# Performance work log

Hardware: AMD Instinct MI355X
Metric: run time of the kernel (lower is better)

The kernel has to match this reference:

```python
import jax, jax.numpy as jnp
import numpy as np
from jax import lax

B, C, D, H, W = 2, 256, 32, 64, 192
TRAIN_W = 640
DISPS = np.arange(D, dtype=np.float32) * 0.01  # norm_disp_range


def conv1x1(x, w, b):
    # x [B,Cin,H,W], w [Cout,Cin]
    return jnp.einsum('bchw,oc->bohw', x, w) + b[None, :, None, None]


def conv3x3(x, w, b):
    y = lax.conv_general_dilated(x, w, (1, 1), 'SAME',
                                 dimension_numbers=('NCHW', 'OIHW', 'NCHW'))
    return y + b[None, :, None, None]


def warp_volume(x, shift_px):
    """Horizontal bilinear warp with border clamp for each disparity.
    x [B,Cc,H,W], shift_px [B,D] (pixel shift) -> [B,Cc,D,H,W]."""
    Wd = x.shape[3]
    j = jnp.arange(Wd, dtype=x.dtype)
    src = jnp.clip(j[None, None, :] + shift_px[:, :, None], 0.0, Wd - 1.0)  # [B,D,W]
    x0 = jnp.floor(src).astype(jnp.int32)
    x1 = jnp.minimum(x0 + 1, Wd - 1)
    frac = src - x0.astype(src.dtype)  # [B,D,W]

    def one(xb, i0, i1, fb):
        g0 = xb[:, :, i0]  # [Cc,H,D,W]
        g1 = xb[:, :, i1]
        out = g0 * (1.0 - fb) + g1 * fb
        return out.transpose(0, 2, 1, 3)  # [Cc,D,H,W]

    return jax.vmap(one)(x, x0, x1, frac)


def setup_inputs() -> dict:
    key = jax.random.key(0)
    ks = jax.random.split(key, 16)
    f32 = jnp.float32
    inp = {
        't_feat': jax.random.normal(ks[0], (B, C, H, W), f32),
        's_feat': jax.random.normal(ks[1], (B, C, H, W), f32),
        'directs': jnp.ones((B, 1, 1, 1), f32),
        'qw': jax.random.normal(ks[2], (C // 4, C), f32) * 0.05,
        'qb': jax.random.normal(ks[3], (C // 4,), f32) * 0.05,
        'kw': jax.random.normal(ks[4], (C // 4, C), f32) * 0.05,
        'kb': jax.random.normal(ks[5], (C // 4,), f32) * 0.05,
        'vw': jax.random.normal(ks[6], (C // 4, C), f32) * 0.05,
        'vb': jax.random.normal(ks[7], (C // 4,), f32) * 0.05,
        'p1w': jax.random.normal(ks[8], (C // 4, C // 2, 3, 3), f32) * 0.05,
        'p1b': jax.random.normal(ks[9], (C // 4,), f32) * 0.05,
        'p2w': jax.random.normal(ks[10], (D, C // 4, 3, 3), f32) * 0.05,
        'p2b': jax.random.normal(ks[11], (D,), f32) * 0.05,
        'rw': jax.random.normal(ks[12], (C, C + D), f32) * 0.05,
        'rb': jax.random.normal(ks[13], (C,), f32) * 0.05,
        'img_w': TRAIN_W,
    }
    return inp


def reference(t_feat, s_feat, directs, qw, qb, kw, kb, vw, vb,
              p1w, p1b, p2w, p2b, rw, rb, img_w):
    rel_scale = (TRAIN_W / img_w) if img_w != TRAIN_W else 1.0
    q = conv1x1(t_feat, qw, qb)  # [B,C/4,H,W]
    k = conv1x1(s_feat, kw, kb)
    v = conv1x1(s_feat, vw, vb)

    Wd = t_feat.shape[3]
    disps = jnp.asarray(DISPS, t_feat.dtype)
    # normalized shift d*2*rel_scale*directs -> pixels: * (W-1)/2
    shift = disps[None, :] * rel_scale * directs.reshape(-1, 1) * (Wd - 1)  # [B,D]

    wk = warp_volume(k, shift)  # [B,C/4,D,H,W]
    wv = warp_volume(v, shift)

    cq = q.shape[1]
    cost = jnp.einsum('bchw,bcdhw->bdhw', q, wk) / (cq ** 0.5)  # [B,D,H,W]
    norm_cost = jax.nn.softmax(cost, axis=1)
    agg_v = jnp.einsum('bdhw,bcdhw->bchw', norm_cost, wv)  # [B,C/4,H,W]

    h1 = jax.nn.elu(conv3x3(jnp.concatenate([q, agg_v], axis=1), p1w, p1b))
    res_cost = conv3x3(h1, p2w, p2b)  # [B,D,H,W]
    cost = (cost + res_cost) * 0.5
    norm_cost = jax.nn.softmax(cost, axis=1)
    x = jax.nn.elu(conv1x1(jnp.concatenate([t_feat, norm_cost], axis=1), rw, rb))
    return x, cost
```

## Files before the change

### kernel.cpp

```cpp
#include <hip/hip_runtime.h>

#define BB 2
#define CC 256
#define CQ 64
#define DD 32
#define HH 64
#define WW 192
#define HW (HH*WW)
#define NPIX (BB*HW)

typedef __attribute__((ext_vector_type(8))) short bf16x8;
typedef __attribute__((ext_vector_type(4))) float f32x4;

__device__ __forceinline__ float b2f(ushort s){ return __uint_as_float(((uint)s)<<16); }
__device__ __forceinline__ ushort f2b(float f){
    uint u = __float_as_uint(f);
    return (ushort)((u + 0x7fffu + ((u>>16)&1u)) >> 16);
}
__device__ __forceinline__ float eluf(float v){ return v > 0.f ? v : (__expf(v)-1.f); }

__global__ __launch_bounds__(256) void k_prep_feat(
    const float* __restrict__ t_feat, const float* __restrict__ s_feat,
    ushort* __restrict__ Tt, ushort* __restrict__ Ts)
{
    __shared__ ushort sT[64*264];
    int blk = blockIdx.x;
    int which = blk / 384;
    int rem   = blk % 384;
    int b     = rem / 192;
    int tile  = rem % 192;
    int p0    = tile*64;
    const float* src = which ? s_feat : t_feat;
    ushort* dst      = which ? Ts : Tt;
    int tid = threadIdx.x;

    for (int i = tid; i < 2048; i += 256){
        int px  = i & 63;
        int c16 = i >> 6;
        const float* p = src + ((size_t)(b*CC + c16*8))*HW + p0 + px;
        uint u[4];
        #pragma unroll
        for (int j2=0;j2<4;++j2)
            u[j2] = (uint)f2b(p[(size_t)(2*j2)*HW]) | ((uint)f2b(p[(size_t)(2*j2+1)*HW])<<16);
        uint4 q4; q4.x=u[0]; q4.y=u[1]; q4.z=u[2]; q4.w=u[3];
        *(uint4*)&sT[(px*33 + c16)*8] = q4;
    }
    __syncthreads();
    for (int i = tid; i < 2048; i += 256){
        int c16 = i & 31;
        int px  = i >> 5;
        uint4 v = *(const uint4*)&sT[(px*33 + c16)*8];
        *(uint4*)(dst + ((size_t)(b*HW + p0 + px))*CC + c16*8) = v;
    }
}

__global__ __launch_bounds__(256) void k_prep_w(
    const float* __restrict__ qw, const float* __restrict__ qb,
    const float* __restrict__ kw, const float* __restrict__ kb,
    const float* __restrict__ vw, const float* __restrict__ vb,
    const float* __restrict__ p1w, const float* __restrict__ p2w,
    const float* __restrict__ rw,
    ushort* __restrict__ Wqkv, float* __restrict__ bqkv,
    ushort* __restrict__ A1, ushort* __restrict__ A2, ushort* __restrict__ Ar)
{
    int id = blockIdx.x*256 + threadIdx.x;
    if (id < 49152) {
        int o = id / 256, c = id % 256;
        float v = (o<64)? qw[o*256+c] : (o<128)? kw[(o-64)*256+c] : vw[(o-128)*256+c];
        Wqkv[id] = f2b(v);
    } else if (id < 49344) {
        int o = id - 49152;
        bqkv[o] = (o<64)? qb[o] : (o<128)? kb[o-64] : vb[o-128];
    } else if (id < 49344+73728) {
        int i = id - 49344;
        int o = i/1152, r = i%1152, t = r/128, ci = r%128;
        A1[i] = f2b(p1w[(size_t)(o*128+ci)*9 + t]);
    } else if (id < 49344+73728+18432) {
        int i = id - (49344+73728);
        int o = i/576, r = i%576, t = r/64, ci = r%64;
        A2[i] = f2b(p2w[(size_t)(o*64+ci)*9 + t]);
    } else if (id < 49344+73728+18432+73728) {
        int i = id - (49344+73728+18432);
        Ar[i] = f2b(rw[i]);
    }
}

__global__ __launch_bounds__(256) void g_qkv(
    const ushort* __restrict__ Tt, const ushort* __restrict__ Ts,
    const ushort* __restrict__ Wqkv, const float* __restrict__ bqkv,
    ushort* __restrict__ X1, ushort* __restrict__ Vb)
{
    __shared__ ushort sT[32*264];
    __shared__ ushort sS[32*264];
    int tid = threadIdx.x;
    int bid = blockIdx.x;
    int tile = (bid & 7)*96 + (bid >> 3);
    int p0 = tile * 32;

    for (int i = tid; i < 1024; i += 256){
        int px = i >> 5, c16 = i & 31;
        size_t gsrc = ((size_t)(p0 + px))*CC + c16*8;
        *(uint4*)&sT[(px*33 + c16)*8] = *(const uint4*)(Tt + gsrc);
        *(uint4*)&sS[(px*33 + c16)*8] = *(const uint4*)(Ts + gsrc);
    }
    __syncthreads();

    int wv = tid >> 6, lane = tid & 63;
    int lm = lane & 15, lk = lane >> 4;
    f32x4 acc[3][2];
    #pragma unroll
    for (int g=0;g<3;++g){ acc[g][0]=(f32x4){0.f,0.f,0.f,0.f}; acc[g][1]=(f32x4){0.f,0.f,0.f,0.f}; }
    const ushort* Ap = Wqkv + (size_t)(wv*16 + lm)*CC + lk*8;

    #pragma unroll
    for (int k0=0; k0<CC; k0+=32){
        bf16x8 a0 = *(const bf16x8*)(Ap + k0);
        bf16x8 a1 = *(const bf16x8*)(Ap + 64*CC + k0);
        bf16x8 a2 = *(const bf16x8*)(Ap + 128*CC + k0);
        #pragma unroll
        for (int nt=0; nt<2; ++nt){
            int ch = (nt*16+lm)*33 + (k0>>3) + lk;
            bf16x8 bT = *(const bf16x8*)&sT[ch*8];
            bf16x8 bS = *(const bf16x8*)&sS[ch*8];
            acc[0][nt] = __builtin_amdgcn_mfma_f32_16x16x32_bf16(a0, bT, acc[0][nt], 0,0,0);
            acc[1][nt] = __builtin_amdgcn_mfma_f32_16x16x32_bf16(a1, bS, acc[1][nt], 0,0,0);
            acc[2][nt] = __builtin_amdgcn_mfma_f32_16x16x32_bf16(a2, bS, acc[2][nt], 0,0,0);
        }
    }
    int ol = wv*16 + lk*4;
    #pragma unroll
    for (int g=0;g<3;++g){
        int ob = g*64 + ol;
        #pragma unroll
        for (int nt=0; nt<2; ++nt){
            int p = p0 + nt*16 + lm;
            uint u0 = (uint)f2b(acc[g][nt][0]+bqkv[ob])   | ((uint)f2b(acc[g][nt][1]+bqkv[ob+1])<<16);
            uint u1 = (uint)f2b(acc[g][nt][2]+bqkv[ob+2]) | ((uint)f2b(acc[g][nt][3]+bqkv[ob+3])<<16);
            ushort* dst;
            if (g==0)      dst = X1 + (size_t)p*128 + ol;
            else if (g==1) dst = X1 + (size_t)p*128 + 64 + ol;
            else           dst = Vb + (size_t)p*64 + ol;
            *(uint2*)dst = make_uint2(u0, u1);
        }
    }
}

#define SVS 193
__global__ __launch_bounds__(512) void k_ca(
    const ushort* __restrict__ X1, const ushort* __restrict__ Vb,
    const float* __restrict__ directs, const int* __restrict__ img_w_p,
    float* __restrict__ C1, ushort* __restrict__ Agg)
{
    __shared__ ushort sK[8*SVS*8];
    __shared__ ushort sV[8*SVS*8];
    int tid = threadIdx.x;
    int j   = blockIdx.x;
    int r8  = j & 7;
    int kk  = j >> 3;
    int sub = kk % 6;
    int rhi = kk / 6;
    int row = rhi*8 + r8;
    int b   = row >> 6;
    int h   = row & 63;
    int w0  = sub * 32;
    size_t rowbase = (size_t)b*HW + (size_t)h*WW;

    for (int i = tid; i < 1536; i += 512){
        int c8 = i & 7, x = i >> 3;
        *(uint4*)&sK[(c8*SVS + x)*8] = *(const uint4*)(X1 + (rowbase+x)*128 + 64 + c8*8);
        *(uint4*)&sV[(c8*SVS + x)*8] = *(const uint4*)(Vb + (rowbase+x)*64 + c8*8);
    }
    __syncthreads();

    int px  = tid >> 4;
    int l16 = tid & 15;
    int oct = l16 >> 1;
    int dh  = l16 & 1;
    int w   = w0 + px;
    size_t n = rowbase + w;

    int imw = img_w_p[0];
    float rel = (imw != 640) ? (640.0f/(float)imw) : 1.0f;
    float sf = 0.01f * rel * directs[b] * 191.0f;
    float wf = (float)w;

    float qf[8];
    {
        bf16x8 qv = *(const bf16x8*)(X1 + n*128 + oct*8);
        #pragma unroll
        for (int j2=0;j2<8;++j2) qf[j2] = b2f((ushort)qv[j2]);
    }

    float cost[16]; int x0k[16]; float frk[16];
    #pragma unroll
    for (int k=0;k<16;++k){
        int d = dh*16 + k;
        float srcx = fminf(fmaxf(wf + (float)d*sf, 0.f), 191.0f);
        int x0 = (int)floorf(srcx);
        int x1 = min(x0+1, 191);
        float fr = srcx - (float)x0;
        x0k[k] = x0; frk[k] = fr;
        bf16x8 k0v = *(const bf16x8*)&sK[(oct*SVS + x0)*8];
        bf16x8 k1v = *(const bf16x8*)&sK[(oct*SVS + x1)*8];
        float s0 = 0.f, s1 = 0.f;
        #pragma unroll
        for (int j2=0;j2<8;++j2){
            s0 += qf[j2]*b2f((ushort)k0v[j2]);
            s1 += qf[j2]*b2f((ushort)k1v[j2]);
        }
        cost[k] = s0 + fr*(s1-s0);
    }
    #pragma unroll
    for (int k=0;k<16;++k){
        float v = cost[k];
        v += __shfl_xor(v, 2);
        v += __shfl_xor(v, 4);
        v += __shfl_xor(v, 8);
        cost[k] = v * 0.125f;
    }
    if (oct == 0){
        float* cp = C1 + n*DD + dh*16;
        #pragma unroll
        for (int q=0;q<4;++q){
            f32x4 t4; t4[0]=cost[q*4]; t4[1]=cost[q*4+1]; t4[2]=cost[q*4+2]; t4[3]=cost[q*4+3];
            *(f32x4*)(cp + q*4) = t4;
        }
    }
    float mm = cost[0];
    #pragma unroll
    for (int k=1;k<16;++k) mm = fmaxf(mm, cost[k]);
    mm = fmaxf(mm, __shfl_xor(mm, 1));
    float ss = 0.f;
    #pragma unroll
    for (int k=0;k<16;++k){ cost[k] = __expf(cost[k]-mm); ss += cost[k]; }
    ss += __shfl_xor(ss, 1);
    float inv = 1.f/ss;

    float agg[8];
    #pragma unroll
    for (int j2=0;j2<8;++j2) agg[j2]=0.f;
    #pragma unroll
    for (int k=0;k<16;++k){
        float pd = cost[k]*inv;
        int x0 = x0k[k];
        int x1 = min(x0+1, 191);
        float fr = frk[k];
        float a1 = pd*fr, a0 = pd - a1;
        bf16x8 v0v = *(const bf16x8*)&sV[(oct*SVS + x0)*8];
        bf16x8 v1v = *(const bf16x8*)&sV[(oct*SVS + x1)*8];
        #pragma unroll
        for (int j2=0;j2<8;++j2)
            agg[j2] += a0*b2f((ushort)v0v[j2]) + a1*b2f((ushort)v1v[j2]);
    }
    #pragma unroll
    for (int j2=0;j2<8;++j2) agg[j2] += __shfl_xor(agg[j2], 1);
    if (dh == 0){
        uint u[4];
        #pragma unroll
        for (int j2=0;j2<4;++j2)
            u[j2] = (uint)f2b(agg[j2*2]) | ((uint)f2b(agg[j2*2+1])<<16);
        uint4 q4; q4.x=u[0]; q4.y=u[1]; q4.z=u[2]; q4.w=u[3];
        *(uint4*)(Agg + n*64 + oct*8) = q4;
    }
}

__global__ __launch_bounds__(256) void g_conv1(
    const ushort* __restrict__ X1, const ushort* __restrict__ Agg,
    const ushort* __restrict__ A1, const float* __restrict__ p1b,
    ushort* __restrict__ X2)
{
    __shared__ ushort sB[3*16*34*8];
    int tid = threadIdx.x;
    int wv = tid >> 6, lane = tid & 63;
    int lm = lane & 15, lk = lane >> 4;
    int bid = blockIdx.x;
    int tile = (bid & 7)*96 + (bid >> 3);
    int n0 = tile * 32;
    int b  = n0 / HW;
    int pl = n0 % HW;
    int h  = pl / WW, w0 = pl % WW;

    for (int i = tid; i < 1632; i += 256){
        int dh = i / 544, rem2 = i % 544;
        int c16 = rem2 / 34, x = rem2 % 34;
        int hh = h + dh - 1, wx = w0 + x - 1;
        uint4 val = make_uint4(0,0,0,0);
        if (hh >= 0 && hh < HH && wx >= 0 && wx < WW){
            size_t pix = (size_t)b*HW + (size_t)hh*WW + wx;
            val = (c16 < 8) ? *(const uint4*)(X1 + pix*128 + c16*8)
                            : *(const uint4*)(Agg + pix*64 + (c16-8)*8);
        }
        *(uint4*)&sB[((dh*16 + c16)*34 + x)*8] = val;
    }
    __syncthreads();

    int mw = wv & 1, nw = wv >> 1;
    const ushort* Ap = A1 + (size_t)(mw*32 + lm)*1152 + lk*8;
    f32x4 acc0 = {0.f,0.f,0.f,0.f}, acc1 = {0.f,0.f,0.f,0.f};
    int xb = nw*16 + lm;
    #pragma unroll
    for (int t=0; t<9; ++t){
        int dh = t/3, dw = t%3;
        #pragma unroll
        for (int c0=0; c0<128; c0+=32){
            bf16x8 bb = *(const bf16x8*)&sB[((dh*16 + (c0>>3)+lk)*34 + xb + dw)*8];
            bf16x8 a0 = *(const bf16x8*)(Ap + t*128 + c0);
            bf16x8 a1 = *(const bf16x8*)(Ap + (size_t)16*1152 + t*128 + c0);
            acc0 = __builtin_amdgcn_mfma_f32_16x16x32_bf16(a0, bb, acc0, 0,0,0);
            acc1 = __builtin_amdgcn_mfma_f32_16x16x32_bf16(a1, bb, acc1, 0,0,0);
        }
    }
    int pg = n0 + nw*16 + lm;
    int o0 = mw*32 + lk*4;
    {
        uint u0 = (uint)f2b(eluf(acc0[0]+p1b[o0]))   | ((uint)f2b(eluf(acc0[1]+p1b[o0+1]))<<16);
        uint u1 = (uint)f2b(eluf(acc0[2]+p1b[o0+2])) | ((uint)f2b(eluf(acc0[3]+p1b[o0+3]))<<16);
        *(uint2*)(X2 + (size_t)pg*64 + o0) = make_uint2(u0, u1);
        int o1 = o0 + 16;
        uint u2 = (uint)f2b(eluf(acc1[0]+p1b[o1]))   | ((uint)f2b(eluf(acc1[1]+p1b[o1+1]))<<16);
        uint u3 = (uint)f2b(eluf(acc1[2]+p1b[o1+2])) | ((uint)f2b(eluf(acc1[3]+p1b[o1+3]))<<16);
        *(uint2*)(X2 + (size_t)pg*64 + o1) = make_uint2(u2, u3);
    }
}

__global__ __launch_bounds__(256) void g_conv2(
    const ushort* __restrict__ X2, const ushort* __restrict__ A2,
    const float* __restrict__ p2b, const float* __restrict__ C1,
    float* __restrict__ cost_out)
{
    __shared__ ushort sB[3*8*34*8];
    int tid = threadIdx.x;
    int wv = tid >> 6, lane = tid & 63;
    int lm = lane & 15, lk = lane >> 4;
    int bid = blockIdx.x;
    int tile = (bid & 7)*96 + (bid >> 3);
    int n0 = tile * 32;
    int b  = n0 / HW;
    int pl = n0 % HW;
    int h  = pl / WW, w0 = pl % WW;

    for (int i = tid; i < 816; i += 256){
        int dh = i / 272, rem2 = i % 272;
        int c16 = rem2 / 34, x = rem2 % 34;
        int hh = h + dh - 1, wx = w0 + x - 1;
        uint4 val = make_uint4(0,0,0,0);
        if (hh >= 0 && hh < HH && wx >= 0 && wx < WW)
            val = *(const uint4*)(X2 + ((size_t)b*HW + (size_t)hh*WW + wx)*64 + c16*8);
        *(uint4*)&sB[((dh*8 + c16)*34 + x)*8] = val;
    }
    __syncthreads();

    int mw = wv & 1, nw = wv >> 1;
    const ushort* Ap = A2 + (size_t)(mw*16 + lm)*576 + lk*8;
    f32x4 acc = {0.f,0.f,0.f,0.f};
    int xb = nw*16 + lm;
    #pragma unroll
    for (int t=0; t<9; ++t){
        int dh = t/3, dw = t%3;
        #pragma unroll
        for (int c0=0; c0<64; c0+=32){
            bf16x8 bb = *(const bf16x8*)&sB[((dh*8 + (c0>>3)+lk)*34 + xb + dw)*8];
            bf16x8 a  = *(const bf16x8*)(Ap + t*64 + c0);
            acc = __builtin_amdgcn_mfma_f32_16x16x32_bf16(a, bb, acc, 0,0,0);
        }
    }
    int pg = n0 + nw*16 + lm;
    int pll = pg % HW;
    int o = mw*16 + lk*4;
    f32x4 cv = *(const f32x4*)(C1 + (size_t)pg*DD + o);
    #pragma unroll
    for (int j=0;j<4;++j)
        cost_out[((size_t)(b*DD + o + j))*HW + pll] = (cv[j] + acc[j] + p2b[o+j]) * 0.5f;
}

__global__ __launch_bounds__(256) void k_sm2(
    const float* __restrict__ cost_out, ushort* __restrict__ NC)
{
    int n = blockIdx.x*256 + threadIdx.x;
    int b = n / HW, pl = n % HW;
    const float* cp = cost_out + (size_t)b*DD*HW + pl;
    float v[DD]; float m = -1e30f;
    #pragma unroll
    for (int d=0; d<DD; ++d){ v[d] = cp[(size_t)d*HW]; m = fmaxf(m, v[d]); }
    float s = 0.f;
    #pragma unroll
    for (int d=0; d<DD; ++d){ v[d] = __expf(v[d]-m); s += v[d]; }
    float inv = 1.f/s;
    ushort* op = NC + (size_t)n*DD;
    #pragma unroll
    for (int d8=0; d8<4; ++d8){
        uint u[4];
        #pragma unroll
        for (int j2=0;j2<4;++j2)
            u[j2] = (uint)f2b(v[d8*8+j2*2]*inv) | ((uint)f2b(v[d8*8+j2*2+1]*inv)<<16);
        uint4 q4; q4.x=u[0]; q4.y=u[1]; q4.z=u[2]; q4.w=u[3];
        *(uint4*)(op + d8*8) = q4;
    }
}

__global__ __launch_bounds__(256) void g_final(
    const ushort* __restrict__ Tt, const ushort* __restrict__ NC,
    const ushort* __restrict__ Ar, const float* __restrict__ rb,
    float* __restrict__ xout)
{
    __shared__ ushort sT[32*264];
    __shared__ ushort sN[32*40];
    int tid = threadIdx.x;
    int bid = blockIdx.x;
    int tile = (bid & 7)*96 + (bid >> 3);
    int p0 = tile * 32;

    for (int i = tid; i < 1024; i += 256){
        int px = i >> 5, c16 = i & 31;
        *(uint4*)&sT[(px*33 + c16)*8] = *(const uint4*)(Tt + ((size_t)(p0+px))*CC + c16*8);
    }
    if (tid < 128){
        int px = tid >> 2, c4 = tid & 3;
        *(uint4*)&sN[(px*5 + c4)*8] = *(const uint4*)(NC + ((size_t)(p0+px))*DD + c4*8);
    }
    __syncthreads();

    int wv = tid >> 6, lane = tid & 63;
    int lm = lane & 15, lk = lane >> 4;
    f32x4 acc[4][2];
    #pragma unroll
    for (int mi=0;mi<4;++mi){ acc[mi][0]=(f32x4){0.f,0.f,0.f,0.f}; acc[mi][1]=(f32x4){0.f,0.f,0.f,0.f}; }
    const ushort* Ap = Ar + (size_t)(wv*64 + lm)*288 + lk*8;

    #pragma unroll
    for (int k0=0; k0<288; k0+=32){
        bf16x8 a[4];
        #pragma unroll
        for (int mi=0;mi<4;++mi) a[mi] = *(const bf16x8*)(Ap + (size_t)mi*16*288 + k0);
        #pragma unroll
        for (int nt=0; nt<2; ++nt){
            int prow = nt*16 + lm;
            bf16x8 bb = (k0 < 256) ? *(const bf16x8*)&sT[(prow*33 + (k0>>3) + lk)*8]
                                   : *(const bf16x8*)&sN[(prow*5 + lk)*8];
            #pragma unroll
            for (int mi=0;mi<4;++mi)
                acc[mi][nt] = __builtin_amdgcn_mfma_f32_16x16x32_bf16(a[mi], bb, acc[mi][nt], 0,0,0);
        }
    }
    #pragma unroll
    for (int mi=0;mi<4;++mi){
        int o = wv*64 + mi*16 + lk*4;
        #pragma unroll
        for (int nt=0; nt<2; ++nt){
            int p = p0 + nt*16 + lm;
            int b = p / HW, pl = p % HW;
            #pragma unroll
            for (int j=0;j<4;++j)
                xout[((size_t)(b*CC + o + j))*HW + pl] = eluf(acc[mi][nt][j] + rb[o+j]);
        }
    }
}

extern "C" void kernel_launch(void* const* d_in, const int* in_sizes, int n_in,
                              void* d_out, int out_size, void* d_ws, size_t ws_size,
                              hipStream_t stream)
{
    const float* t_feat = (const float*)d_in[0];
    const float* s_feat = (const float*)d_in[1];
    const float* directs= (const float*)d_in[2];
    const float* qw = (const float*)d_in[3];
    const float* qb = (const float*)d_in[4];
    const float* kw = (const float*)d_in[5];
    const float* kb = (const float*)d_in[6];
    const float* vw = (const float*)d_in[7];
    const float* vb = (const float*)d_in[8];
    const float* p1w= (const float*)d_in[9];
    const float* p1b= (const float*)d_in[10];
    const float* p2w= (const float*)d_in[11];
    const float* p2b= (const float*)d_in[12];
    const float* rw = (const float*)d_in[13];
    const float* rb = (const float*)d_in[14];
    const int* img_w= (const int*)d_in[15];

    char* wsb = (char*)d_ws;
    ushort* Tt   = (ushort*)(wsb + 0);
    char*  tsreg = wsb + 12582912;
    ushort* Ts   = (ushort*)tsreg;
    ushort* X2   = (ushort*)tsreg;
    float*  C1   = (float*)(tsreg + 3145728);
    ushort* Agg  = (ushort*)(tsreg + 6291456);
    ushort* X1   = (ushort*)(wsb + 25165824);
    ushort* Vb   = (ushort*)(wsb + 31457280);
    ushort* NC   = (ushort*)(wsb + 31457280);
    ushort* Wqkv = (ushort*)(wsb + 34603008);
    float*  bqkv = (float*) (wsb + 34701312);
    ushort* A1   = (ushort*)(wsb + 34702336);
    ushort* A2   = (ushort*)(wsb + 34849792);
    ushort* Ar   = (ushort*)(wsb + 34886656);
    if (ws_size < 35034112) return;

    float* xout     = (float*)d_out;
    float* cost_out = xout + (size_t)BB*CC*HW;

    k_prep_feat<<<768, 256, 0, stream>>>(t_feat, s_feat, Tt, Ts);
    k_prep_w  <<<841,  256, 0, stream>>>(qw,qb,kw,kb,vw,vb,p1w,p2w,rw, Wqkv,bqkv,A1,A2,Ar);
    g_qkv     <<<768,  256, 0, stream>>>(Tt, Ts, Wqkv, bqkv, X1, Vb);
    k_ca      <<<768,  512, 0, stream>>>(X1, Vb, directs, img_w, C1, Agg);
    g_conv1   <<<768,  256, 0, stream>>>(X1, Agg, A1, p1b, X2);
    g_conv2   <<<768,  256, 0, stream>>>(X2, A2, p2b, C1, cost_out);
    k_sm2     <<<96,   256, 0, stream>>>(cost_out, NC);
    g_final   <<<768,  256, 0, stream>>>(Tt, NC, Ar, rb, xout);
}
```

Measured before the change: 113.4 us.

## Recast cost-volume attention as banded MFMA matmuls with scattered warp weights

The k_ca kernel now loads only a 160-column band of K and V around each 32-pixel tile into swizzled shared memory. It computes a dense Q·K score matrix with bf16 MFMA and interpolates cost per disparity from that matrix. Softmax weights are scattered via shared-memory atomics into a per-pixel column-weight matrix, and a second MFMA multiplies V by those weights to form the aggregate. This replaces scalar per-disparity dot products with matrix-core work, at the cost of extra syncs, atomics and redundant work on unused band columns. Clamping indices into the band assumes shifts stay within the band, which holds for the default disparity range.

```diff
diff --git a/kernel.cpp b/kernel.cpp
--- a/kernel.cpp
+++ b/kernel.cpp
@@ -145,14 +145,19 @@
     }
 }
 
-#define SVS 193
+#define BAND 160
+#define SROW 161
+#define PROW 168
 __global__ __launch_bounds__(512) void k_ca(
     const ushort* __restrict__ X1, const ushort* __restrict__ Vb,
     const float* __restrict__ directs, const int* __restrict__ img_w_p,
     float* __restrict__ C1, ushort* __restrict__ Agg)
 {
-    __shared__ ushort sK[8*SVS*8];
-    __shared__ ushort sV[8*SVS*8];
+    __shared__ ushort sQ[32*64];
+    __shared__ ushort sK[BAND*64];
+    __shared__ ushort sV[BAND*64];
+    __shared__ float  sS[32*SROW];
+    __shared__ ushort sPC[32*PROW];
     int tid = threadIdx.x;
     int j   = blockIdx.x;
     int r8  = j & 7;
@@ -165,102 +170,126 @@
     int w0  = sub * 32;
     size_t rowbase = (size_t)b*HW + (size_t)h*WW;
 
-    for (int i = tid; i < 1536; i += 512){
-        int c8 = i & 7, x = i >> 3;
-        *(uint4*)&sK[(c8*SVS + x)*8] = *(const uint4*)(X1 + (rowbase+x)*128 + 64 + c8*8);
-        *(uint4*)&sV[(c8*SVS + x)*8] = *(const uint4*)(Vb + (rowbase+x)*64 + c8*8);
+    for (int i = tid; i < BAND*8; i += 512){
+        int x = i >> 3, c8 = i & 7;
+        int gx = w0 - 64 + x;
+        uint4 kv = make_uint4(0,0,0,0), vv = make_uint4(0,0,0,0);
+        if (gx >= 0 && gx < WW){
+            kv = *(const uint4*)(X1 + (rowbase+gx)*128 + 64 + c8*8);
+            vv = *(const uint4*)(Vb + (rowbase+gx)*64 + c8*8);
+        }
+        int sw = (x*8 + (c8 ^ (x&7)))*8;
+        *(uint4*)&sK[sw] = kv;
+        *(uint4*)&sV[sw] = vv;
+    }
+    if (tid < 256){
+        int px = tid >> 3, c8 = tid & 7;
+        uint4 qv = *(const uint4*)(X1 + (rowbase + w0 + px)*128 + c8*8);
+        *(uint4*)&sQ[(px*8 + (c8 ^ (px&7)))*8] = qv;
+    }
+    __syncthreads();
+
+    int w8 = tid >> 6, lane = tid & 63;
+    int lm = lane & 15, lk = lane >> 4;
+
+    {
+        int mt = w8 & 1;
+        int qrow = mt*16 + lm;
+        for (int nt = (w8 >> 1); nt < 10; nt += 4){
+            int xrow = nt*16 + lm;
+            f32x4 acc = {0.f,0.f,0.f,0.f};
+            #pragma unroll
+            for (int kt=0; kt<2; ++kt){
+                bf16x8 a = *(const bf16x8*)&sQ[(qrow*8 + ((kt*4+lk) ^ (qrow&7)))*8];
+                bf16x8 bbf = *(const bf16x8*)&sK[(xrow*8 + ((kt*4+lk) ^ (xrow&7)))*8];
+                acc = __builtin_amdgcn_mfma_f32_16x16x32_bf16(a, bbf, acc, 0,0,0);
+            }
+            #pragma unroll
+            for (int jj=0; jj<4; ++jj)
+                sS[(mt*16 + lk*4 + jj)*SROW + xrow] = acc[jj];
+        }
     }
     __syncthreads();
 
     int px  = tid >> 4;
     int l16 = tid & 15;
-    int oct = l16 >> 1;
-    int dh  = l16 & 1;
     int w   = w0 + px;
     size_t n = rowbase + w;
-
     int imw = img_w_p[0];
     float rel = (imw != 640) ? (640.0f/(float)imw) : 1.0f;
     float sf = 0.01f * rel * directs[b] * 191.0f;
     float wf = (float)w;
 
-    float qf[8];
-    {
-        bf16x8 qv = *(const bf16x8*)(X1 + n*128 + oct*8);
-        #pragma unroll
-        for (int j2=0;j2<8;++j2) qf[j2] = b2f((ushort)qv[j2]);
-    }
-
-    float cost[16]; int x0k[16]; float frk[16];
-    #pragma unroll
-    for (int k=0;k<16;++k){
-        int d = dh*16 + k;
+    float cost[2]; int xi0[2], xi1[2]; float frk[2];
+    #pragma unroll
+    for (int t=0; t<2; ++t){
+        int d = l16*2 + t;
         float srcx = fminf(fmaxf(wf + (float)d*sf, 0.f), 191.0f);
         int x0 = (int)floorf(srcx);
-        int x1 = min(x0+1, 191);
+        int x1 = min(x0+1, WW-1);
         float fr = srcx - (float)x0;
-        x0k[k] = x0; frk[k] = fr;
-        bf16x8 k0v = *(const bf16x8*)&sK[(oct*SVS + x0)*8];
-        bf16x8 k1v = *(const bf16x8*)&sK[(oct*SVS + x1)*8];
-        float s0 = 0.f, s1 = 0.f;
-        #pragma unroll
-        for (int j2=0;j2<8;++j2){
-            s0 += qf[j2]*b2f((ushort)k0v[j2]);
-            s1 += qf[j2]*b2f((ushort)k1v[j2]);
-        }
-        cost[k] = s0 + fr*(s1-s0);
-    }
-    #pragma unroll
-    for (int k=0;k<16;++k){
-        float v = cost[k];
-        v += __shfl_xor(v, 2);
-        v += __shfl_xor(v, 4);
-        v += __shfl_xor(v, 8);
-        cost[k] = v * 0.125f;
-    }
-    if (oct == 0){
-        float* cp = C1 + n*DD + dh*16;
-        #pragma unroll
-        for (int q=0;q<4;++q){
-            f32x4 t4; t4[0]=cost[q*4]; t4[1]=cost[q*4+1]; t4[2]=cost[q*4+2]; t4[3]=cost[q*4+3];
-            *(f32x4*)(cp + q*4) = t4;
-        }
-    }
-    float mm = cost[0];
-    #pragma unroll
-    for (int k=1;k<16;++k) mm = fmaxf(mm, cost[k]);
+        int i0 = min(max(x0 - w0 + 64, 0), BAND-1);
+        int i1 = min(max(x1 - w0 + 64, 0), BAND-1);
+        xi0[t] = i0; xi1[t] = i1; frk[t] = fr;
+        float s0 = sS[px*SROW + i0];
+        float s1 = sS[px*SROW + i1];
+        cost[t] = (s0 + fr*(s1-s0)) * 0.125f;
+    }
+    *(float2*)(C1 + n*DD + l16*2) = make_float2(cost[0], cost[1]);
+    float mm = fmaxf(cost[0], cost[1]);
     mm = fmaxf(mm, __shfl_xor(mm, 1));
-    float ss = 0.f;
-    #pragma unroll
-    for (int k=0;k<16;++k){ cost[k] = __expf(cost[k]-mm); ss += cost[k]; }
+    mm = fmaxf(mm, __shfl_xor(mm, 2));
+    mm = fmaxf(mm, __shfl_xor(mm, 4));
+    mm = fmaxf(mm, __shfl_xor(mm, 8));
+    float e0 = __expf(cost[0]-mm), e1 = __expf(cost[1]-mm);
+    float ss = e0 + e1;
     ss += __shfl_xor(ss, 1);
+    ss += __shfl_xor(ss, 2);
+    ss += __shfl_xor(ss, 4);
+    ss += __shfl_xor(ss, 8);
     float inv = 1.f/ss;
-
-    float agg[8];
-    #pragma unroll
-    for (int j2=0;j2<8;++j2) agg[j2]=0.f;
-    #pragma unroll
-    for (int k=0;k<16;++k){
-        float pd = cost[k]*inv;
-        int x0 = x0k[k];
-        int x1 = min(x0+1, 191);
-        float fr = frk[k];
-        float a1 = pd*fr, a0 = pd - a1;
-        bf16x8 v0v = *(const bf16x8*)&sV[(oct*SVS + x0)*8];
-        bf16x8 v1v = *(const bf16x8*)&sV[(oct*SVS + x1)*8];
-        #pragma unroll
-        for (int j2=0;j2<8;++j2)
-            agg[j2] += a0*b2f((ushort)v0v[j2]) + a1*b2f((ushort)v1v[j2]);
-    }
-    #pragma unroll
-    for (int j2=0;j2<8;++j2) agg[j2] += __shfl_xor(agg[j2], 1);
-    if (dh == 0){
-        uint u[4];
-        #pragma unroll
-        for (int j2=0;j2<4;++j2)
-            u[j2] = (uint)f2b(agg[j2*2]) | ((uint)f2b(agg[j2*2+1])<<16);
-        uint4 q4; q4.x=u[0]; q4.y=u[1]; q4.z=u[2]; q4.w=u[3];
-        *(uint4*)(Agg + n*64 + oct*8) = q4;
+    float p0 = e0*inv, p1 = e1*inv;
+    __syncthreads();
+
+    for (int i = tid; i < 32*SROW; i += 512) sS[i] = 0.f;
+    __syncthreads();
+
+    {
+        float w1a = p0*frk[0], w0a = p0 - w1a;
+        float w1b = p1*frk[1], w0b = p1 - w1b;
+        atomicAdd(&sS[px*SROW + xi0[0]], w0a);
+        atomicAdd(&sS[px*SROW + xi1[0]], w1a);
+        atomicAdd(&sS[px*SROW + xi0[1]], w0b);
+        atomicAdd(&sS[px*SROW + xi1[1]], w1b);
+    }
+    __syncthreads();
+
+    #pragma unroll
+    for (int q=0; q<10; ++q){
+        int xi = l16 + q*16;
+        sPC[px*PROW + xi] = f2b(sS[px*SROW + xi]);
+    }
+    __syncthreads();
+
+    {
+        int mi = w8 & 3;
+        int ni = w8 >> 2;
+        int c  = mi*16 + lm;
+        int wr = ni*16 + lm;
+        f32x4 acc = {0.f,0.f,0.f,0.f};
+        for (int kt=0; kt<5; ++kt){
+            bf16x8 a;
+            #pragma unroll
+            for (int jj=0; jj<8; ++jj){
+                int x = kt*32 + lk*8 + jj;
+                a[jj] = (short)sV[(x*8 + ((c>>3) ^ (x&7)))*8 + (c&7)];
+            }
+            bf16x8 bbf = *(const bf16x8*)&sPC[wr*PROW + kt*32 + lk*8];
+            acc = __builtin_amdgcn_mfma_f32_16x16x32_bf16(a, bbf, acc, 0,0,0);
+        }
+        uint u0 = (uint)f2b(acc[0]) | ((uint)f2b(acc[1])<<16);
+        uint u1 = (uint)f2b(acc[2]) | ((uint)f2b(acc[3])<<16);
+        *(uint2*)(Agg + (rowbase + w0 + wr)*64 + mi*16 + lk*4) = make_uint2(u0, u1);
     }
 }
 
```

After: 112.9 us. Within noise of the previous version (-0.4%).
